# Kernel tuning notes

Hardware: AMD Instinct MI355X
Metric: run time of the kernel (lower is better)

Reference implementation:

```python
import jax, jax.numpy as jnp
import numpy as np

N_NODES = 100000
N_EDGES = 1600000
IN, HID, OUT = 128, 256, 64
EPS = 0.0  # init_eps=0, learn_eps=False


def setup_inputs() -> dict:
    key = jax.random.key(0)
    k1, k2, k3, k4, k5 = jax.random.split(key, 5)
    x = jax.random.normal(k1, (N_NODES, IN), dtype=jnp.float32)
    edge_src = jax.random.randint(k2, (N_EDGES,), 0, N_NODES, dtype=jnp.int64)
    edge_dst = jax.random.randint(k3, (N_EDGES,), 0, N_NODES, dtype=jnp.int64)
    W1 = jax.random.normal(k4, (IN, HID), dtype=jnp.float32) * (1.0 / np.sqrt(IN))
    W2 = jax.random.normal(k5, (HID, OUT), dtype=jnp.float32) * (1.0 / np.sqrt(HID))
    return {"x": x, "edge_src": edge_src, "edge_dst": edge_dst, "W1": W1, "W2": W2}


def _gin_conv(h, edge_src, edge_dst, W, n_nodes):
    # sum aggregation of messages h[src] into dst, then (1+eps)*h + agg, then linear (no bias)
    agg = jax.ops.segment_sum(h[edge_src], edge_dst, num_segments=n_nodes)
    return ((1.0 + EPS) * h + agg) @ W


def reference(x, edge_src, edge_dst, W1, W2):
    n = x.shape[0]
    h = _gin_conv(x, edge_src, edge_dst, W1, n)   # [N, HID]
    h = _gin_conv(h, edge_src, edge_dst, W2, n)   # [N, OUT]
    return h
```

## Files before the change

### kernel.cpp

```cpp
#include <hip/hip_runtime.h>
#include <hip/hip_bf16.h>

#define IN_F  128
#define HID_F 256
#define OUT_F 64
#define BUCKET_SHIFT 9
#define BUCKET_SZ 512
#define EPB 4096
#define CAP 10240

typedef __attribute__((ext_vector_type(8))) short bf16x8;
typedef __attribute__((ext_vector_type(4))) float f32x4;

__device__ __forceinline__ float bf2f(unsigned short u) {
    union { unsigned int i; float f; } v; v.i = ((unsigned int)u) << 16; return v.f;
}
__device__ __forceinline__ float bf2f_lo(unsigned int p) {
    union { unsigned int i; float f; } v; v.i = p << 16; return v.f;
}
__device__ __forceinline__ float bf2f_hi(unsigned int p) {
    union { unsigned int i; float f; } v; v.i = p & 0xffff0000u; return v.f;
}
__device__ __forceinline__ unsigned short f2bf(float f) {
    __hip_bfloat16 b = __float2bfloat16(f);
    return *reinterpret_cast<unsigned short*>(&b);
}

__global__ __launch_bounds__(1024) void k_front_bin(
    const float* __restrict__ x, unsigned short* __restrict__ xb, long long total8,
    const float* __restrict__ W1, const float* __restrict__ W2,
    unsigned short* __restrict__ w12s,
    const int* __restrict__ esrc, const int* __restrict__ edst,
    int* __restrict__ gcur, unsigned int* __restrict__ binned,
    int nEdges, int xBlocks)
{
    __shared__ int hist[256];
    __shared__ int lcur[256];
    int bid = blockIdx.x;
    int t = threadIdx.x;
    if (bid < xBlocks) {
        long long i = (long long)bid * 1024 + t;
        if (i >= total8) return;
        const float4* p = reinterpret_cast<const float4*>(x) + i * 2;
        float4 a = p[0], b = p[1];
        ushort4 o0, o1;
        o0.x = f2bf(a.x); o0.y = f2bf(a.y); o0.z = f2bf(a.z); o0.w = f2bf(a.w);
        o1.x = f2bf(b.x); o1.y = f2bf(b.y); o1.z = f2bf(b.z); o1.w = f2bf(b.w);
        reinterpret_cast<ushort4*>(xb)[i * 2]     = o0;
        reinterpret_cast<ushort4*>(xb)[i * 2 + 1] = o1;
    } else if (bid < xBlocks + 8) {
        int idx = (bid - xBlocks) * 1024 + t;
        int c = idx >> 9, L = (idx >> 3) & 63, j = idx & 7;
        int nt = c >> 2, ks = c & 3;
        int k = ks * 32 + (L >> 4) * 8 + j;
        int n = nt * 16 + (L & 15);
        float s = 0.f;
        #pragma unroll 8
        for (int jj = 0; jj < HID_F; ++jj)
            s += W1[k * HID_F + jj] * W2[jj * OUT_F + n];
        w12s[idx] = f2bf(s);
    } else {
        int bb = bid - xBlocks - 8;
        if (t < 256) hist[t] = 0;
        __syncthreads();
        long long base = (long long)bb * EPB;
        #pragma unroll
        for (int k = 0; k < EPB / 1024; ++k) {
            long long e = base + k * 1024 + t;
            if (e < nEdges) atomicAdd(&hist[edst[e] >> BUCKET_SHIFT], 1);
        }
        __syncthreads();
        if (t < 256) {
            int h = hist[t];
            lcur[t] = (h > 0) ? atomicAdd(&gcur[t], h) : 0;
        }
        __syncthreads();
        #pragma unroll
        for (int k = 0; k < EPB / 1024; ++k) {
            long long e = base + k * 1024 + t;
            if (e < nEdges) {
                int s = esrc[e], d = edst[e];
                int b = d >> BUCKET_SHIFT;
                int pos = atomicAdd(&lcur[b], 1);
                binned[(size_t)b * CAP + pos] =
                    (((unsigned int)(d & (BUCKET_SZ - 1))) << 23) | (unsigned int)s;
            }
        }
    }
}

__global__ __launch_bounds__(512) void k_localcsr(
    const unsigned int* __restrict__ binned, const int* __restrict__ gcur,
    int* __restrict__ rowbeg, int* __restrict__ rowend,
    int* __restrict__ eidx, int nNodes)
{
    __shared__ int ldeg[BUCKET_SZ];
    __shared__ int lscan[BUCKET_SZ];
    int t = threadIdx.x;
    ldeg[t] = 0;
    __syncthreads();
    int eb0 = blockIdx.x * CAP;
    int cnt = gcur[blockIdx.x];
    int node0 = blockIdx.x << BUCKET_SHIFT;
    for (int e = t; e < cnt; e += 512)
        atomicAdd(&ldeg[binned[eb0 + e] >> 23], 1);
    __syncthreads();
    int s = ldeg[t];
    lscan[t] = s;
    __syncthreads();
    for (int d = 1; d < 512; d <<= 1) {
        int add = (t >= d) ? lscan[t - d] : 0;
        __syncthreads();
        lscan[t] += add;
        __syncthreads();
    }
    int excl = lscan[t] - s;
    int n0 = node0 + t;
    if (n0 < nNodes) { rowbeg[n0] = eb0 + excl; rowend[n0] = eb0 + excl + s; }
    __syncthreads();
    ldeg[t] = excl;
    __syncthreads();
    for (int e = t; e < cnt; e += 512) {
        unsigned int p = binned[eb0 + e];
        int dl = (int)(p >> 23), sv = (int)(p & 0x7fffffu);
        int pos = atomicAdd(&ldeg[dl], 1);
        eidx[eb0 + pos] = sv;
    }
}

__global__ __launch_bounds__(1024) void gather1z(
    const unsigned short* __restrict__ xb, const int* __restrict__ rowbeg,
    const int* __restrict__ rowend, const int* __restrict__ eidx,
    const unsigned short* __restrict__ w12s,
    unsigned short* __restrict__ z, int nNodes)
{
    __shared__ unsigned short aggT[64 * IN_F];
    int wave = threadIdx.x >> 6, lane = threadIdx.x & 63;
    int m0 = blockIdx.x * 64;
    int g = lane >> 4;
    int f = lane & 15;
    char* scb = reinterpret_cast<char*>(aggT);

    for (int j = 0; j < 4; ++j) {
        int r = wave * 4 + j;
        int n = m0 + r;
        char* sc = scb + ((r >> 4) << 12);
        int lr = r & 15;
        int wb = ((lr << 8) + (f << 4)) ^ ((lr & 7) << 4);
        if (n < nNodes) {
            int beg = __builtin_amdgcn_readfirstlane(rowbeg[n]);
            int end = __builtin_amdgcn_readfirstlane(rowend[n]);
            float acc[8] = {0.f, 0.f, 0.f, 0.f, 0.f, 0.f, 0.f, 0.f};
            for (int e0 = beg; e0 < end; e0 += 64) {
                int cnt = min(64, end - e0);
                int e = (lane < cnt) ? eidx[e0 + lane] : 0;
                for (int i = 0; i < cnt; i += 16) {
                    uint4 v[4];
                    unsigned int vmask[4];
                    #pragma unroll
                    for (int jj = 0; jj < 4; ++jj) {
                        int eij = i + 4 * jj + g;
                        int src = __builtin_amdgcn_ds_bpermute(eij << 2, e);
                        int s0  = __builtin_amdgcn_readlane(e, i + 4 * jj);
                        bool valid = eij < cnt;
                        vmask[jj] = valid ? 0xffffffffu : 0u;
                        src = valid ? src : s0;
                        v[jj] = *reinterpret_cast<const uint4*>(
                            xb + (unsigned)src * IN_F + (f << 3));
                    }
                    #pragma unroll
                    for (int jj = 0; jj < 4; ++jj) {
                        unsigned int a0 = v[jj].x & vmask[jj], a1 = v[jj].y & vmask[jj];
                        unsigned int a2 = v[jj].z & vmask[jj], a3 = v[jj].w & vmask[jj];
                        acc[0] += bf2f_lo(a0); acc[1] += bf2f_hi(a0);
                        acc[2] += bf2f_lo(a1); acc[3] += bf2f_hi(a1);
                        acc[4] += bf2f_lo(a2); acc[5] += bf2f_hi(a2);
                        acc[6] += bf2f_lo(a3); acc[7] += bf2f_hi(a3);
                    }
                }
            }
            #pragma unroll
            for (int k = 0; k < 8; ++k) {
                acc[k] += __shfl_xor(acc[k], 16);
                acc[k] += __shfl_xor(acc[k], 32);
            }
            uint4 sv = *reinterpret_cast<const uint4*>(xb + (size_t)n * IN_F + (f << 3));
            acc[0] += bf2f_lo(sv.x); acc[1] += bf2f_hi(sv.x);
            acc[2] += bf2f_lo(sv.y); acc[3] += bf2f_hi(sv.y);
            acc[4] += bf2f_lo(sv.z); acc[5] += bf2f_hi(sv.z);
            acc[6] += bf2f_lo(sv.w); acc[7] += bf2f_hi(sv.w);
            if (g == 0) {
                uint4 o;
                o.x = (unsigned int)f2bf(acc[0]) | ((unsigned int)f2bf(acc[1]) << 16);
                o.y = (unsigned int)f2bf(acc[2]) | ((unsigned int)f2bf(acc[3]) << 16);
                o.z = (unsigned int)f2bf(acc[4]) | ((unsigned int)f2bf(acc[5]) << 16);
                o.w = (unsigned int)f2bf(acc[6]) | ((unsigned int)f2bf(acc[7]) << 16);
                *reinterpret_cast<uint4*>(sc + wb) = o;
            }
        } else {
            if (g == 0) *reinterpret_cast<uint4*>(sc + wb) = make_uint4(0, 0, 0, 0);
        }
    }
    __syncthreads();

    {
        int tile = wave >> 2, nt = wave & 3;
        char* sc = scb + (tile << 12);
        int row = lane & 15, quad = lane >> 4;
        f32x4 acc2 = {};
        const bf16x8* bBase = reinterpret_cast<const bf16x8*>(w12s) + lane;
        #pragma unroll
        for (int ks = 0; ks < 4; ++ks) {
            int ab = ((row << 8) + (quad << 4) + (ks << 6)) ^ ((row & 7) << 4);
            bf16x8 a = *reinterpret_cast<const bf16x8*>(sc + ab);
            bf16x8 b = bBase[(nt * 4 + ks) * 64];
            acc2 = __builtin_amdgcn_mfma_f32_16x16x32_bf16(a, b, acc2, 0, 0, 0);
        }
        int mt = m0 + tile * 16;
        size_t outBase = (size_t)(mt + quad * 4) * OUT_F + nt * 16 + row;
        #pragma unroll
        for (int i = 0; i < 4; ++i) {
            if (mt + quad * 4 + i >= nNodes) break;
            z[outBase + (size_t)i * OUT_F] = f2bf(acc2[i]);
        }
    }
}

__global__ __launch_bounds__(256) void gather2(
    const unsigned short* __restrict__ z, const int* __restrict__ rowbeg,
    const int* __restrict__ rowend,
    const int* __restrict__ eidx, float* __restrict__ out, int nNodes)
{
    int n    = blockIdx.x * 4 + __builtin_amdgcn_readfirstlane(threadIdx.x >> 6);
    int lane = threadIdx.x & 63;
    if (n >= nNodes) return;
    int beg = __builtin_amdgcn_readfirstlane(rowbeg[n]);
    int end = __builtin_amdgcn_readfirstlane(rowend[n]);
    int g = lane >> 3;
    int f = lane & 7;
    float acc[8] = {0.f, 0.f, 0.f, 0.f, 0.f, 0.f, 0.f, 0.f};

    for (int e0 = beg; e0 < end; e0 += 64) {
        int cnt = min(64, end - e0);
        int e = (lane < cnt) ? eidx[e0 + lane] : 0;
        for (int i = 0; i < cnt; i += 32) {
            uint4 v[4];
            unsigned int vmask[4];
            #pragma unroll
            for (int j = 0; j < 4; ++j) {
                int eij = i + 8 * j + g;
                int src = __builtin_amdgcn_ds_bpermute(eij << 2, e);
                int s0  = __builtin_amdgcn_readlane(e, i + 8 * j);
                bool valid = eij < cnt;
                vmask[j] = valid ? 0xffffffffu : 0u;
                src = valid ? src : s0;
                v[j] = *reinterpret_cast<const uint4*>(
                    z + (unsigned)src * OUT_F + (f << 3));
            }
            #pragma unroll
            for (int j = 0; j < 4; ++j) {
                unsigned int a0 = v[j].x & vmask[j], a1 = v[j].y & vmask[j];
                unsigned int a2 = v[j].z & vmask[j], a3 = v[j].w & vmask[j];
                acc[0] += bf2f_lo(a0); acc[1] += bf2f_hi(a0);
                acc[2] += bf2f_lo(a1); acc[3] += bf2f_hi(a1);
                acc[4] += bf2f_lo(a2); acc[5] += bf2f_hi(a2);
                acc[6] += bf2f_lo(a3); acc[7] += bf2f_hi(a3);
            }
        }
    }
    #pragma unroll
    for (int k = 0; k < 8; ++k) {
        acc[k] += __shfl_xor(acc[k], 8);
        acc[k] += __shfl_xor(acc[k], 16);
        acc[k] += __shfl_xor(acc[k], 32);
    }
    uint4 sv = *reinterpret_cast<const uint4*>(z + (size_t)n * OUT_F + (f << 3));
    acc[0] += bf2f_lo(sv.x); acc[1] += bf2f_hi(sv.x);
    acc[2] += bf2f_lo(sv.y); acc[3] += bf2f_hi(sv.y);
    acc[4] += bf2f_lo(sv.z); acc[5] += bf2f_hi(sv.z);
    acc[6] += bf2f_lo(sv.w); acc[7] += bf2f_hi(sv.w);
    if (g == 0) {
        float* o = out + (size_t)n * OUT_F + (f << 3);
        *reinterpret_cast<float4*>(o)     = make_float4(acc[0], acc[1], acc[2], acc[3]);
        *reinterpret_cast<float4*>(o + 4) = make_float4(acc[4], acc[5], acc[6], acc[7]);
    }
}

extern "C" void kernel_launch(void* const* d_in, const int* in_sizes, int n_in,
                              void* d_out, int out_size, void* d_ws, size_t ws_size,
                              hipStream_t stream) {
    const float* x  = (const float*)d_in[0];
    const int* esrc = (const int*)d_in[1];
    const int* edst = (const int*)d_in[2];
    const float* W1 = (const float*)d_in[3];
    const float* W2 = (const float*)d_in[4];
    float* out      = (float*)d_out;

    const int nNodes = in_sizes[0] / IN_F;
    const int nEdges = in_sizes[1];
    const int NB = (nNodes + BUCKET_SZ - 1) / BUCKET_SZ;
    const int A  = (nEdges + EPB - 1) / EPB;

    char* ws = (char*)d_ws;
    size_t off = 0;
    auto alloc = [&](size_t bytes) {
        char* p = ws + off; off = (off + bytes + 63) & ~(size_t)63; return p;
    };
    unsigned short* xb  = (unsigned short*)alloc((size_t)nNodes * IN_F * 2);
    unsigned short* z   = (unsigned short*)alloc((size_t)nNodes * OUT_F * 2);
    unsigned int* binned = (unsigned int*)alloc((size_t)NB * CAP * 4);
    int* eidx           = (int*)alloc((size_t)NB * CAP * 4);
    unsigned short* w12s = (unsigned short*)alloc((size_t)IN_F * OUT_F * 2);
    int* rowbeg         = (int*)alloc((size_t)nNodes * 4);
    int* rowend         = (int*)alloc((size_t)nNodes * 4);
    int* gcur           = (int*)alloc(256 * 4);

    hipMemsetAsync(gcur, 0, 256 * 4, stream);

    long long total8 = (long long)nNodes * IN_F / 8;
    const int xBlocks = (int)((total8 + 1023) / 1024);
    k_front_bin<<<xBlocks + 8 + A, 1024, 0, stream>>>(
        x, xb, total8, W1, W2, w12s, esrc, edst, gcur, binned, nEdges, xBlocks);

    k_localcsr<<<NB, 512, 0, stream>>>(binned, gcur, rowbeg, rowend, eidx, nNodes);

    const int g1Blocks = (nNodes + 63) / 64;
    const int nBlocks = (nNodes + 3) / 4;
    gather1z<<<g1Blocks, 1024, 0, stream>>>(xb, rowbeg, rowend, eidx, w12s, z, nNodes);
    gather2<<<nBlocks, 256, 0, stream>>>(z, rowbeg, rowend, eidx, out, nNodes);
}
```

Baseline: 262.4 us.

## Project x to 64 features before aggregation so both gathers use narrow rows

Uses linearity of the combined W1·W2 transform: the projection y = x·W12 is computed first with an MFMA GEMM that reads fp32 x directly, and then two 64-wide gather-sum passes run on y. Before this, the first gather read 128-wide bf16 rows. The separate x-to-bf16 conversion pass and the shared-memory staging in gather1z go away. The cost is one extra kernel launch and an extra 64-wide bf16 intermediate buffer, plus bf16 rounding at a different point in the computation.

```diff
diff --git a/kernel.cpp b/kernel.cpp
--- a/kernel.cpp
+++ b/kernel.cpp
@@ -27,29 +27,18 @@
 }
 
 __global__ __launch_bounds__(1024) void k_front_bin(
-    const float* __restrict__ x, unsigned short* __restrict__ xb, long long total8,
     const float* __restrict__ W1, const float* __restrict__ W2,
     unsigned short* __restrict__ w12s,
     const int* __restrict__ esrc, const int* __restrict__ edst,
     int* __restrict__ gcur, unsigned int* __restrict__ binned,
-    int nEdges, int xBlocks)
+    int nEdges)
 {
     __shared__ int hist[256];
     __shared__ int lcur[256];
     int bid = blockIdx.x;
     int t = threadIdx.x;
-    if (bid < xBlocks) {
-        long long i = (long long)bid * 1024 + t;
-        if (i >= total8) return;
-        const float4* p = reinterpret_cast<const float4*>(x) + i * 2;
-        float4 a = p[0], b = p[1];
-        ushort4 o0, o1;
-        o0.x = f2bf(a.x); o0.y = f2bf(a.y); o0.z = f2bf(a.z); o0.w = f2bf(a.w);
-        o1.x = f2bf(b.x); o1.y = f2bf(b.y); o1.z = f2bf(b.z); o1.w = f2bf(b.w);
-        reinterpret_cast<ushort4*>(xb)[i * 2]     = o0;
-        reinterpret_cast<ushort4*>(xb)[i * 2 + 1] = o1;
-    } else if (bid < xBlocks + 8) {
-        int idx = (bid - xBlocks) * 1024 + t;
+    if (bid < 8) {
+        int idx = bid * 1024 + t;
         int c = idx >> 9, L = (idx >> 3) & 63, j = idx & 7;
         int nt = c >> 2, ks = c & 3;
         int k = ks * 32 + (L >> 4) * 8 + j;
@@ -60,7 +49,7 @@
             s += W1[k * HID_F + jj] * W2[jj * OUT_F + n];
         w12s[idx] = f2bf(s);
     } else {
-        int bb = bid - xBlocks - 8;
+        int bb = bid - 8;
         if (t < 256) hist[t] = 0;
         __syncthreads();
         long long base = (long long)bb * EPB;
@@ -128,108 +117,47 @@
     }
 }
 
-__global__ __launch_bounds__(1024) void gather1z(
-    const unsigned short* __restrict__ xb, const int* __restrict__ rowbeg,
-    const int* __restrict__ rowend, const int* __restrict__ eidx,
-    const unsigned short* __restrict__ w12s,
-    unsigned short* __restrict__ z, int nNodes)
-{
-    __shared__ unsigned short aggT[64 * IN_F];
+__global__ __launch_bounds__(256) void y_gemm(
+    const float* __restrict__ x, const unsigned short* __restrict__ w12s,
+    unsigned short* __restrict__ y, int nNodes)
+{
     int wave = threadIdx.x >> 6, lane = threadIdx.x & 63;
-    int m0 = blockIdx.x * 64;
-    int g = lane >> 4;
-    int f = lane & 15;
-    char* scb = reinterpret_cast<char*>(aggT);
-
-    for (int j = 0; j < 4; ++j) {
-        int r = wave * 4 + j;
-        int n = m0 + r;
-        char* sc = scb + ((r >> 4) << 12);
-        int lr = r & 15;
-        int wb = ((lr << 8) + (f << 4)) ^ ((lr & 7) << 4);
-        if (n < nNodes) {
-            int beg = __builtin_amdgcn_readfirstlane(rowbeg[n]);
-            int end = __builtin_amdgcn_readfirstlane(rowend[n]);
-            float acc[8] = {0.f, 0.f, 0.f, 0.f, 0.f, 0.f, 0.f, 0.f};
-            for (int e0 = beg; e0 < end; e0 += 64) {
-                int cnt = min(64, end - e0);
-                int e = (lane < cnt) ? eidx[e0 + lane] : 0;
-                for (int i = 0; i < cnt; i += 16) {
-                    uint4 v[4];
-                    unsigned int vmask[4];
-                    #pragma unroll
-                    for (int jj = 0; jj < 4; ++jj) {
-                        int eij = i + 4 * jj + g;
-                        int src = __builtin_amdgcn_ds_bpermute(eij << 2, e);
-                        int s0  = __builtin_amdgcn_readlane(e, i + 4 * jj);
-                        bool valid = eij < cnt;
-                        vmask[jj] = valid ? 0xffffffffu : 0u;
-                        src = valid ? src : s0;
-                        v[jj] = *reinterpret_cast<const uint4*>(
-                            xb + (unsigned)src * IN_F + (f << 3));
-                    }
-                    #pragma unroll
-                    for (int jj = 0; jj < 4; ++jj) {
-                        unsigned int a0 = v[jj].x & vmask[jj], a1 = v[jj].y & vmask[jj];
-                        unsigned int a2 = v[jj].z & vmask[jj], a3 = v[jj].w & vmask[jj];
-                        acc[0] += bf2f_lo(a0); acc[1] += bf2f_hi(a0);
-                        acc[2] += bf2f_lo(a1); acc[3] += bf2f_hi(a1);
-                        acc[4] += bf2f_lo(a2); acc[5] += bf2f_hi(a2);
-                        acc[6] += bf2f_lo(a3); acc[7] += bf2f_hi(a3);
-                    }
-                }
-            }
-            #pragma unroll
-            for (int k = 0; k < 8; ++k) {
-                acc[k] += __shfl_xor(acc[k], 16);
-                acc[k] += __shfl_xor(acc[k], 32);
-            }
-            uint4 sv = *reinterpret_cast<const uint4*>(xb + (size_t)n * IN_F + (f << 3));
-            acc[0] += bf2f_lo(sv.x); acc[1] += bf2f_hi(sv.x);
-            acc[2] += bf2f_lo(sv.y); acc[3] += bf2f_hi(sv.y);
-            acc[4] += bf2f_lo(sv.z); acc[5] += bf2f_hi(sv.z);
-            acc[6] += bf2f_lo(sv.w); acc[7] += bf2f_hi(sv.w);
-            if (g == 0) {
-                uint4 o;
-                o.x = (unsigned int)f2bf(acc[0]) | ((unsigned int)f2bf(acc[1]) << 16);
-                o.y = (unsigned int)f2bf(acc[2]) | ((unsigned int)f2bf(acc[3]) << 16);
-                o.z = (unsigned int)f2bf(acc[4]) | ((unsigned int)f2bf(acc[5]) << 16);
-                o.w = (unsigned int)f2bf(acc[6]) | ((unsigned int)f2bf(acc[7]) << 16);
-                *reinterpret_cast<uint4*>(sc + wb) = o;
-            }
-        } else {
-            if (g == 0) *reinterpret_cast<uint4*>(sc + wb) = make_uint4(0, 0, 0, 0);
-        }
-    }
-    __syncthreads();
-
-    {
-        int tile = wave >> 2, nt = wave & 3;
-        char* sc = scb + (tile << 12);
-        int row = lane & 15, quad = lane >> 4;
-        f32x4 acc2 = {};
-        const bf16x8* bBase = reinterpret_cast<const bf16x8*>(w12s) + lane;
+    int m0 = blockIdx.x * 64 + wave * 16;
+    if (m0 >= nNodes) return;
+    int row = lane & 15, quad = lane >> 4;
+    int rr = min(m0 + row, nNodes - 1);
+    const float* aRow = x + (size_t)rr * IN_F + quad * 8;
+    f32x4 acc[4] = {};
+    const bf16x8* bBase = reinterpret_cast<const bf16x8*>(w12s) + lane;
+    #pragma unroll
+    for (int ks = 0; ks < 4; ++ks) {
+        float4 a0 = *reinterpret_cast<const float4*>(aRow + ks * 32);
+        float4 a1 = *reinterpret_cast<const float4*>(aRow + ks * 32 + 4);
+        bf16x8 a;
+        a[0] = (short)f2bf(a0.x); a[1] = (short)f2bf(a0.y);
+        a[2] = (short)f2bf(a0.z); a[3] = (short)f2bf(a0.w);
+        a[4] = (short)f2bf(a1.x); a[5] = (short)f2bf(a1.y);
+        a[6] = (short)f2bf(a1.z); a[7] = (short)f2bf(a1.w);
         #pragma unroll
-        for (int ks = 0; ks < 4; ++ks) {
-            int ab = ((row << 8) + (quad << 4) + (ks << 6)) ^ ((row & 7) << 4);
-            bf16x8 a = *reinterpret_cast<const bf16x8*>(sc + ab);
+        for (int nt = 0; nt < 4; ++nt) {
             bf16x8 b = bBase[(nt * 4 + ks) * 64];
-            acc2 = __builtin_amdgcn_mfma_f32_16x16x32_bf16(a, b, acc2, 0, 0, 0);
-        }
-        int mt = m0 + tile * 16;
-        size_t outBase = (size_t)(mt + quad * 4) * OUT_F + nt * 16 + row;
+            acc[nt] = __builtin_amdgcn_mfma_f32_16x16x32_bf16(a, b, acc[nt], 0, 0, 0);
+        }
+    }
+    size_t outBase = (size_t)(m0 + quad * 4) * OUT_F + row;
+    #pragma unroll
+    for (int i = 0; i < 4; ++i) {
+        if (m0 + quad * 4 + i >= nNodes) break;
         #pragma unroll
-        for (int i = 0; i < 4; ++i) {
-            if (mt + quad * 4 + i >= nNodes) break;
-            z[outBase + (size_t)i * OUT_F] = f2bf(acc2[i]);
-        }
-    }
-}
-
-__global__ __launch_bounds__(256) void gather2(
-    const unsigned short* __restrict__ z, const int* __restrict__ rowbeg,
+        for (int nt = 0; nt < 4; ++nt)
+            y[outBase + (size_t)i * OUT_F + nt * 16] = f2bf(acc[nt][i]);
+    }
+}
+
+__global__ __launch_bounds__(256) void gather1y(
+    const unsigned short* __restrict__ y, const int* __restrict__ rowbeg,
     const int* __restrict__ rowend,
-    const int* __restrict__ eidx, float* __restrict__ out, int nNodes)
+    const int* __restrict__ eidx, unsigned short* __restrict__ aggy, int nNodes)
 {
     int n    = blockIdx.x * 4 + __builtin_amdgcn_readfirstlane(threadIdx.x >> 6);
     int lane = threadIdx.x & 63;
@@ -255,7 +183,7 @@
                 vmask[j] = valid ? 0xffffffffu : 0u;
                 src = valid ? src : s0;
                 v[j] = *reinterpret_cast<const uint4*>(
-                    z + (unsigned)src * OUT_F + (f << 3));
+                    y + (unsigned)src * OUT_F + (f << 3));
             }
             #pragma unroll
             for (int j = 0; j < 4; ++j) {
@@ -274,7 +202,70 @@
         acc[k] += __shfl_xor(acc[k], 16);
         acc[k] += __shfl_xor(acc[k], 32);
     }
-    uint4 sv = *reinterpret_cast<const uint4*>(z + (size_t)n * OUT_F + (f << 3));
+    uint4 sv = *reinterpret_cast<const uint4*>(y + (size_t)n * OUT_F + (f << 3));
+    acc[0] += bf2f_lo(sv.x); acc[1] += bf2f_hi(sv.x);
+    acc[2] += bf2f_lo(sv.y); acc[3] += bf2f_hi(sv.y);
+    acc[4] += bf2f_lo(sv.z); acc[5] += bf2f_hi(sv.z);
+    acc[6] += bf2f_lo(sv.w); acc[7] += bf2f_hi(sv.w);
+    if (g == 0) {
+        uint4 o;
+        o.x = (unsigned int)f2bf(acc[0]) | ((unsigned int)f2bf(acc[1]) << 16);
+        o.y = (unsigned int)f2bf(acc[2]) | ((unsigned int)f2bf(acc[3]) << 16);
+        o.z = (unsigned int)f2bf(acc[4]) | ((unsigned int)f2bf(acc[5]) << 16);
+        o.w = (unsigned int)f2bf(acc[6]) | ((unsigned int)f2bf(acc[7]) << 16);
+        *reinterpret_cast<uint4*>(aggy + (size_t)n * OUT_F + (f << 3)) = o;
+    }
+}
+
+__global__ __launch_bounds__(256) void gather2(
+    const unsigned short* __restrict__ aggy, const int* __restrict__ rowbeg,
+    const int* __restrict__ rowend,
+    const int* __restrict__ eidx, float* __restrict__ out, int nNodes)
+{
+    int n    = blockIdx.x * 4 + __builtin_amdgcn_readfirstlane(threadIdx.x >> 6);
+    int lane = threadIdx.x & 63;
+    if (n >= nNodes) return;
+    int beg = __builtin_amdgcn_readfirstlane(rowbeg[n]);
+    int end = __builtin_amdgcn_readfirstlane(rowend[n]);
+    int g = lane >> 3;
+    int f = lane & 7;
+    float acc[8] = {0.f, 0.f, 0.f, 0.f, 0.f, 0.f, 0.f, 0.f};
+
+    for (int e0 = beg; e0 < end; e0 += 64) {
+        int cnt = min(64, end - e0);
+        int e = (lane < cnt) ? eidx[e0 + lane] : 0;
+        for (int i = 0; i < cnt; i += 32) {
+            uint4 v[4];
+            unsigned int vmask[4];
+            #pragma unroll
+            for (int j = 0; j < 4; ++j) {
+                int eij = i + 8 * j + g;
+                int src = __builtin_amdgcn_ds_bpermute(eij << 2, e);
+                int s0  = __builtin_amdgcn_readlane(e, i + 8 * j);
+                bool valid = eij < cnt;
+                vmask[j] = valid ? 0xffffffffu : 0u;
+                src = valid ? src : s0;
+                v[j] = *reinterpret_cast<const uint4*>(
+                    aggy + (unsigned)src * OUT_F + (f << 3));
+            }
+            #pragma unroll
+            for (int j = 0; j < 4; ++j) {
+                unsigned int a0 = v[j].x & vmask[j], a1 = v[j].y & vmask[j];
+                unsigned int a2 = v[j].z & vmask[j], a3 = v[j].w & vmask[j];
+                acc[0] += bf2f_lo(a0); acc[1] += bf2f_hi(a0);
+                acc[2] += bf2f_lo(a1); acc[3] += bf2f_hi(a1);
+                acc[4] += bf2f_lo(a2); acc[5] += bf2f_hi(a2);
+                acc[6] += bf2f_lo(a3); acc[7] += bf2f_hi(a3);
+            }
+        }
+    }
+    #pragma unroll
+    for (int k = 0; k < 8; ++k) {
+        acc[k] += __shfl_xor(acc[k], 8);
+        acc[k] += __shfl_xor(acc[k], 16);
+        acc[k] += __shfl_xor(acc[k], 32);
+    }
+    uint4 sv = *reinterpret_cast<const uint4*>(aggy + (size_t)n * OUT_F + (f << 3));
     acc[0] += bf2f_lo(sv.x); acc[1] += bf2f_hi(sv.x);
     acc[2] += bf2f_lo(sv.y); acc[3] += bf2f_hi(sv.y);
     acc[4] += bf2f_lo(sv.z); acc[5] += bf2f_hi(sv.z);
@@ -306,26 +297,25 @@
     auto alloc = [&](size_t bytes) {
         char* p = ws + off; off = (off + bytes + 63) & ~(size_t)63; return p;
     };
-    unsigned short* xb  = (unsigned short*)alloc((size_t)nNodes * IN_F * 2);
-    unsigned short* z   = (unsigned short*)alloc((size_t)nNodes * OUT_F * 2);
+    unsigned short* y    = (unsigned short*)alloc((size_t)nNodes * OUT_F * 2);
+    unsigned short* aggy = (unsigned short*)alloc((size_t)nNodes * OUT_F * 2);
     unsigned int* binned = (unsigned int*)alloc((size_t)NB * CAP * 4);
-    int* eidx           = (int*)alloc((size_t)NB * CAP * 4);
+    int* eidx            = (int*)alloc((size_t)NB * CAP * 4);
     unsigned short* w12s = (unsigned short*)alloc((size_t)IN_F * OUT_F * 2);
-    int* rowbeg         = (int*)alloc((size_t)nNodes * 4);
-    int* rowend         = (int*)alloc((size_t)nNodes * 4);
-    int* gcur           = (int*)alloc(256 * 4);
+    int* rowbeg          = (int*)alloc((size_t)nNodes * 4);
+    int* rowend          = (int*)alloc((size_t)nNodes * 4);
+    int* gcur            = (int*)alloc(256 * 4);
 
     hipMemsetAsync(gcur, 0, 256 * 4, stream);
 
-    long long total8 = (long long)nNodes * IN_F / 8;
-    const int xBlocks = (int)((total8 + 1023) / 1024);
-    k_front_bin<<<xBlocks + 8 + A, 1024, 0, stream>>>(
-        x, xb, total8, W1, W2, w12s, esrc, edst, gcur, binned, nEdges, xBlocks);
+    k_front_bin<<<8 + A, 1024, 0, stream>>>(
+        W1, W2, w12s, esrc, edst, gcur, binned, nEdges);
 
     k_localcsr<<<NB, 512, 0, stream>>>(binned, gcur, rowbeg, rowend, eidx, nNodes);
 
-    const int g1Blocks = (nNodes + 63) / 64;
+    const int mBlocks = (nNodes + 63) / 64;
     const int nBlocks = (nNodes + 3) / 4;
-    gather1z<<<g1Blocks, 1024, 0, stream>>>(xb, rowbeg, rowend, eidx, w12s, z, nNodes);
-    gather2<<<nBlocks, 256, 0, stream>>>(z, rowbeg, rowend, eidx, out, nNodes);
-}
+    y_gemm<<<mBlocks, 256, 0, stream>>>(x, w12s, y, nNodes);
+    gather1y<<<nBlocks, 256, 0, stream>>>(y, rowbeg, rowend, eidx, aggy, nNodes);
+    gather2<<<nBlocks, 256, 0, stream>>>(aggy, rowbeg, rowend, eidx, out, nNodes);
+}
```

After: 244.3 us. -6.9%, faster.
